# Optimization experiments

Hardware: AMD Instinct MI355X
Metric: run time of the kernel (lower is better)

The kernel has to match this reference:

```python
import jax, jax.numpy as jnp
import numpy as np

FREQ_DIM = 64
BLOCK_DIM = 64
N = 256          # lattice sites
CH = 6           # channel_num -> block diagonals at offsets -1, 0, +1
S = 2 * 16 + CH - 2   # seq_num = 36
BS = 4           # block_size (kron of two 2x2 matrices)
HID = 128
EPS = 1e-5
B = 32

_e = np.eye(2)
_sx = np.array([[0., 1.], [1., 0.]])
_siy = np.array([[0., 1.], [-1., 0.]])
_sz = np.array([[1., 0.], [0., -1.]])
_p = [_e, _sx, _siy, _sz]
KRONS = jnp.asarray(np.stack([np.kron(_p[a], _p[b]) for a in range(4) for b in range(4)]).astype(np.float32))  # (16,4,4)
Z1 = KRONS[12]  # kron(sigma_z, I) used for interaction blocks ('z1')


def _bn(h, g, b):
    # BatchNorm1d in training mode: biased batch statistics over axis 0
    mu = h.mean(axis=0)
    v = h.var(axis=0)
    return g * (h - mu) / jnp.sqrt(v + EPS) + b


def _mlp(x, Win, bin_, Wmid, bmid, Wout, bout, gamma, beta):
    # depth-4 MLP: Lin+ReLU, then (BN,Lin,ReLU) x2, then BN,Lin,ReLU
    h = jax.nn.relu(x @ Win + bin_)
    for i in range(Wmid.shape[0]):
        h = jax.nn.relu(_bn(h, gamma[i], beta[i]) @ Wmid[i] + bmid[i])
    return jax.nn.relu(_bn(h, gamma[-1], beta[-1]) @ Wout + bout)


def _lstm(xs, h0, c0, Wih, Whh, bih, bhh):
    # xs: (B, T, S); torch gate order i, f, g, o
    def step(carry, x_t):
        h, c = carry
        gates = x_t @ Wih.T + h @ Whh.T + (bih + bhh)
        i, f, g, o = jnp.split(gates, 4, axis=-1)
        c = jax.nn.sigmoid(f) * c + jax.nn.sigmoid(i) * jnp.tanh(g)
        h = jax.nn.sigmoid(o) * jnp.tanh(c)
        return (h, c), h
    _, hs = jax.lax.scan(step, (h0, c0), jnp.swapaxes(xs, 0, 1))
    return jnp.swapaxes(hs, 0, 1)


def setup_inputs() -> dict:
    key = jax.random.key(0)
    ks = iter(jax.random.split(key, 48))
    def w(shape, s=0.05):
        return jax.random.normal(next(ks), shape, dtype=jnp.float32) * s
    d = {
        'x': w((B, FREQ_DIM + BLOCK_DIM), 1.0),
        'fd_Win': w((FREQ_DIM, HID)), 'fd_bin': w((HID,)),
        'fd_Wmid': w((2, HID, HID)), 'fd_bmid': w((2, HID)),
        'fd_Wout': w((HID, S)), 'fd_bout': w((S,)),
        'fd_gamma': jnp.ones((3, HID), jnp.float32), 'fd_beta': jnp.zeros((3, HID), jnp.float32),
        'bd_Win': w((BLOCK_DIM, HID)), 'bd_bin': w((HID,)),
        'bd_Wmid': w((2, HID, HID)), 'bd_bmid': w((2, HID)),
        'bd_Wout': w((HID, S)), 'bd_bout': w((S,)),
        'bd_gamma': jnp.ones((3, HID), jnp.float32), 'bd_beta': jnp.zeros((3, HID), jnp.float32),
        'sc_Win': w((S, 1, HID)), 'sc_bin': w((S, HID)),
        'sc_Wmid': w((S, 2, HID, HID)), 'sc_bmid': w((S, 2, HID)),
        'sc_Wout': w((S, HID, N)), 'sc_bout': w((S, N)),
        'sc_gamma': jnp.ones((S, 3, HID), jnp.float32), 'sc_beta': jnp.zeros((S, 3, HID), jnp.float32),
        'lstm_Wih': w((4 * S, S)), 'lstm_Whh': w((4 * S, S)),
        'lstm_bih': w((4 * S,)), 'lstm_bhh': w((4 * S,)),
        'mix_W': w((S, 2 * S)), 'mix_b': w((S,)),
    }
    return d


def reference(x, fd_Win, fd_bin, fd_Wmid, fd_bmid, fd_Wout, fd_bout, fd_gamma, fd_beta,
              bd_Win, bd_bin, bd_Wmid, bd_bmid, bd_Wout, bd_bout, bd_gamma, bd_beta,
              sc_Win, sc_bin, sc_Wmid, sc_bmid, sc_Wout, sc_bout, sc_gamma, sc_beta,
              lstm_Wih, lstm_Whh, lstm_bih, lstm_bhh, mix_W, mix_b):
    Bsz = x.shape[0]
    block = _mlp(x[:, FREQ_DIM:], bd_Win, bd_bin, bd_Wmid, bd_bmid, bd_Wout, bd_bout, bd_gamma, bd_beta)  # (B,S)
    freq = _mlp(x[:, :FREQ_DIM], fd_Win, fd_bin, fd_Wmid, fd_bmid, fd_Wout, fd_bout, fd_gamma, fd_beta)   # (B,S)
    # S independent scalar->N MLPs, batched with vmap over the stacked params
    sc = jax.vmap(_mlp)(freq.T[:, :, None], sc_Win, sc_bin, sc_Wmid, sc_bmid,
                        sc_Wout, sc_bout, sc_gamma, sc_beta)  # (S,B,N)
    freq_seq = jnp.cos(sc).transpose(1, 2, 0)   # (B,N,S)
    seq = _lstm(freq_seq, block, jnp.zeros_like(block), lstm_Wih, lstm_Whh, lstm_bih, lstm_bhh)  # (B,N,S)
    block_seq = jnp.concatenate([jnp.broadcast_to(block[:, :, None], (Bsz, S, N)),
                                 jnp.swapaxes(seq, 1, 2)], axis=1)  # (B,2S,N)
    # 1x1 Conv2d == channel mixing matmul
    mixed = jnp.einsum('bcn,oc->bon', block_seq, mix_W) + mix_b[None, :, None]  # (B,S,N)
    inter = mixed[:, :CH - 2]                          # (B,CH-2,N)
    onsite = mixed[:, CH - 2:].reshape(Bsz, 2, 16, N)  # (B,2,16,N)
    H_int = jnp.einsum('bcn,ij->bcnij', inter, Z1)         # (B,CH-2,N,4,4)
    H_os = jnp.einsum('bgkn,kij->bgnij', onsite, KRONS)    # (B,2,N,4,4) summed over 16 pairs
    half = (CH - 2) // 2
    strips = jnp.concatenate([H_int[:, :half], H_os, H_int[:, half:]], axis=1)  # (B,CH,N,4,4)
    strips = strips.reshape(Bsz, CH // 2, 2, N, BS, BS)
    # banded block assembly: strip i lives on block-diagonal offset i - (CH//2)//2
    grid = jnp.zeros((Bsz, 2, N, N, BS, BS), dtype=x.dtype)
    for i in range(CH // 2):
        o = i - (CH // 2) // 2
        rows = jnp.arange(N - abs(o)) + max(0, -o)
        cols = rows + o
        grid = grid.at[:, :, rows, cols].set(strips[:, i][:, :, rows])
    matrix = grid.transpose(0, 1, 2, 4, 3, 5).reshape(Bsz, 2, N * BS, N * BS)
    return matrix
```

## Files before the change

kernel.cpp:

```cpp
#include <hip/hip_runtime.h>
#include <math.h>

#define EPSF 1e-5f

__device__ __forceinline__ float tanhf_fast(float x) {
    return 1.f - 2.f / (__expf(2.f * x) + 1.f);
}

__device__ void mlp64_body(const float* __restrict__ xin,
                           const float* __restrict__ Win,
                           const float* __restrict__ bin_,
                           const float* __restrict__ Wmid,
                           const float* __restrict__ bmid,
                           const float* __restrict__ Wout,
                           const float* __restrict__ bout,
                           const float* __restrict__ gamma,
                           const float* __restrict__ beta,
                           float* __restrict__ out)
{
    __shared__ float sX[32 * 64];
    __shared__ float sA[32 * 128];
    __shared__ float sB[32 * 128];
    __shared__ float sMu[128], sRs[128];
    int tid = threadIdx.x;

    for (int idx = tid; idx < 32 * 64; idx += 256) {
        int b = idx >> 6, c = idx & 63;
        sX[idx] = xin[b * 128 + c];
    }
    __syncthreads();

    for (int idx = tid; idx < 32 * 128; idx += 256) {
        int b = idx >> 7, j = idx & 127;
        float acc = bin_[j];
        for (int c = 0; c < 64; ++c) acc = fmaf(sX[b * 64 + c], Win[c * 128 + j], acc);
        sA[idx] = fmaxf(acc, 0.f);
    }
    __syncthreads();

    float* cur = sA;
    float* nxt = sB;
    for (int l = 0; l < 3; ++l) {
        if (tid < 128) {
            float s = 0.f, s2 = 0.f;
            for (int b = 0; b < 32; ++b) {
                float v = cur[b * 128 + tid];
                s += v; s2 += v * v;
            }
            float mu = s * (1.f / 32.f);
            float var = s2 * (1.f / 32.f) - mu * mu;
            sMu[tid] = mu;
            sRs[tid] = rsqrtf(var + EPSF);
        }
        __syncthreads();
        for (int idx = tid; idx < 32 * 128; idx += 256) {
            int j = idx & 127;
            cur[idx] = gamma[l * 128 + j] * (cur[idx] - sMu[j]) * sRs[j] + beta[l * 128 + j];
        }
        __syncthreads();
        if (l < 2) {
            for (int idx = tid; idx < 32 * 128; idx += 256) {
                int b = idx >> 7, j = idx & 127;
                float acc = bmid[l * 128 + j];
                for (int c = 0; c < 128; ++c)
                    acc = fmaf(cur[b * 128 + c], Wmid[(l * 128 + c) * 128 + j], acc);
                nxt[idx] = fmaxf(acc, 0.f);
            }
            __syncthreads();
            float* t = cur; cur = nxt; nxt = t;
        } else {
            for (int idx = tid; idx < 32 * 36; idx += 256) {
                int b = idx / 36, j = idx - b * 36;
                float acc = bout[j];
                for (int c = 0; c < 128; ++c)
                    acc = fmaf(cur[b * 128 + c], Wout[c * 36 + j], acc);
                out[idx] = fmaxf(acc, 0.f);
            }
        }
    }
}

__global__ __launch_bounds__(256) void k_mlp2(
    const float* __restrict__ x,
    const float* fdWin, const float* fdbin, const float* fdWmid, const float* fdbmid,
    const float* fdWout, const float* fdbout, const float* fdg, const float* fdbt,
    const float* bdWin, const float* bdbin, const float* bdWmid, const float* bdbmid,
    const float* bdWout, const float* bdbout, const float* bdg, const float* bdbt,
    float* freq, float* blk)
{
    if (blockIdx.x == 0)
        mlp64_body(x + 64, bdWin, bdbin, bdWmid, bdbmid, bdWout, bdbout, bdg, bdbt, blk);
    else
        mlp64_body(x, fdWin, fdbin, fdWmid, fdbmid, fdWout, fdbout, fdg, fdbt, freq);
}

__global__ __launch_bounds__(512) void k_sc(
    const float* __restrict__ freq,
    const float* __restrict__ Win,
    const float* __restrict__ bin_,
    const float* __restrict__ Wmid,
    const float* __restrict__ bmid,
    const float* __restrict__ Wout,
    const float* __restrict__ bout,
    const float* __restrict__ gamma,
    const float* __restrict__ beta,
    float* __restrict__ fseq)
{
    int s = blockIdx.x, tid = threadIdx.x;
    __shared__ float sA[32 * 128];
    __shared__ float sB[32 * 128];
    __shared__ float sMu[128], sRs[128];
    const float* Wm = Wmid + (size_t)s * 2 * 128 * 128;
    const float* Wo = Wout + (size_t)s * 128 * 256;
    const float* gm = gamma + s * 3 * 128;
    const float* bt = beta + s * 3 * 128;

    for (int idx = tid; idx < 32 * 128; idx += 512) {
        int b = idx >> 7, j = idx & 127;
        float acc = fmaf(freq[b * 36 + s], Win[s * 128 + j], bin_[s * 128 + j]);
        sA[idx] = fmaxf(acc, 0.f);
    }
    __syncthreads();

    float* cur = sA;
    float* nxt = sB;
    for (int l = 0; l < 3; ++l) {
        if (tid < 128) {
            float sm = 0.f, s2 = 0.f;
            for (int b = 0; b < 32; ++b) {
                float v = cur[b * 128 + tid];
                sm += v; s2 += v * v;
            }
            float mu = sm * (1.f / 32.f);
            float var = s2 * (1.f / 32.f) - mu * mu;
            sMu[tid] = mu;
            sRs[tid] = rsqrtf(var + EPSF);
        }
        __syncthreads();
        for (int idx = tid; idx < 32 * 128; idx += 512) {
            int j = idx & 127;
            cur[idx] = gm[l * 128 + j] * (cur[idx] - sMu[j]) * sRs[j] + bt[l * 128 + j];
        }
        __syncthreads();
        if (l < 2) {
            for (int idx = tid; idx < 32 * 128; idx += 512) {
                int b = idx >> 7, j = idx & 127;
                float acc = bmid[(s * 2 + l) * 128 + j];
                for (int c = 0; c < 128; ++c)
                    acc = fmaf(cur[b * 128 + c], Wm[(l * 128 + c) * 128 + j], acc);
                nxt[idx] = fmaxf(acc, 0.f);
            }
            __syncthreads();
            float* t = cur; cur = nxt; nxt = t;
        } else {
            for (int idx = tid; idx < 32 * 256; idx += 512) {
                int b = idx >> 8, n = idx & 255;
                float acc = bout[s * 256 + n];
                for (int c = 0; c < 128; ++c)
                    acc = fmaf(cur[b * 128 + c], Wo[c * 256 + n], acc);
                float v = fmaxf(acc, 0.f);
                fseq[((size_t)n * 32 + b) * 36 + s] = cosf(v);
            }
        }
    }
}

__global__ __launch_bounds__(512) void k_xg(
    const float* __restrict__ fseq, const float* __restrict__ Wih,
    const float* __restrict__ bih, const float* __restrict__ bhh,
    float* __restrict__ Xg)
{
    int t = blockIdx.x, tid = threadIdx.x;
    __shared__ float sF[32 * 36];
    for (int idx = tid; idx < 1152; idx += 512) sF[idx] = fseq[(size_t)t * 1152 + idx];
    __syncthreads();
    for (int idx = tid; idx < 32 * 144; idx += 512) {
        int b = idx / 144, j = idx - b * 144;
        float acc = bih[j] + bhh[j];
        #pragma unroll
        for (int s2 = 0; s2 < 36; ++s2)
            acc = fmaf(sF[b * 36 + s2], Wih[j * 36 + s2], acc);
        Xg[((size_t)t * 32 + b) * 144 + j] = acc;
    }
}

__global__ __launch_bounds__(192) void k_lstm(
    const float* __restrict__ Xg, const float* __restrict__ blockIn,
    const float* __restrict__ Whh, float* __restrict__ hseq)
{
    int b = blockIdx.x, tid = threadIdx.x;
    __shared__ float sh[36];
    __shared__ float sg[144];
    float w[36];
    if (tid < 144) {
        #pragma unroll
        for (int k = 0; k < 36; ++k) w[k] = Whh[tid * 36 + k];
    }
    if (tid < 36) sh[tid] = blockIn[b * 36 + tid];
    float c = 0.f;
    float xg = (tid < 144) ? Xg[(size_t)b * 144 + tid] : 0.f;
    const int type = tid / 36;
    __syncthreads();

    for (int t = 0; t < 256; ++t) {
        float act = 0.f;
        if (tid < 144) {
            float a0 = 0.f, a1 = 0.f, a2 = 0.f, a3 = 0.f;
            #pragma unroll
            for (int k = 0; k < 36; k += 4) {
                a0 = fmaf(w[k + 0], sh[k + 0], a0);
                a1 = fmaf(w[k + 1], sh[k + 1], a1);
                a2 = fmaf(w[k + 2], sh[k + 2], a2);
                a3 = fmaf(w[k + 3], sh[k + 3], a3);
            }
            float gate = xg + (a0 + a1) + (a2 + a3);
            float sarg = (type == 2) ? 2.f * gate : gate;
            float sv = 1.f / (1.f + __expf(-sarg));
            act = (type == 2) ? 2.f * sv - 1.f : sv;
        }
        if (t < 255 && tid < 144) xg = Xg[((size_t)(t + 1) * 32 + b) * 144 + tid];
        if (tid < 144) sg[tid] = act;
        __syncthreads();
        if (tid < 36) {
            float iv = sg[tid], fv = sg[36 + tid], gv = sg[72 + tid], ov = sg[108 + tid];
            c = fmaf(fv, c, iv * gv);
            float h = ov * tanhf_fast(c);
            sh[tid] = h;
            hseq[((size_t)b * 256 + t) * 36 + tid] = h;
        }
        __syncthreads();
    }
}

__global__ __launch_bounds__(256) void k_mixed(
    const float* __restrict__ blockIn, const float* __restrict__ hseq,
    const float* __restrict__ mixW, const float* __restrict__ mixb,
    float* __restrict__ mixed)
{
    int wg = blockIdx.x;
    int b = wg / 36, o = wg - b * 36;
    int n = threadIdx.x;
    float acc = mixb[o];
    const float* wrow = mixW + o * 72;
    const float* blk = blockIn + b * 36;
    #pragma unroll
    for (int c = 0; c < 36; ++c) acc = fmaf(wrow[c], blk[c], acc);
    const float* hp = hseq + ((size_t)b * 256 + n) * 36;
    #pragma unroll
    for (int u = 0; u < 36; ++u) acc = fmaf(wrow[36 + u], hp[u], acc);
    mixed[(size_t)wg * 256 + n] = acc;
}

__device__ __forceinline__ float pauliv(int p, int r, int c) {
    switch (p) {
        case 0: return (r == c) ? 1.f : 0.f;
        case 1: return (r != c) ? 1.f : 0.f;
        case 2: return (r == 0 && c == 1) ? 1.f : ((r == 1 && c == 0) ? -1.f : 0.f);
        default: return (r == c) ? ((r == 0) ? 1.f : -1.f) : 0.f;
    }
}

__global__ __launch_bounds__(256) void k_asm(
    const float* __restrict__ mixed, float* __restrict__ out)
{
    int wg = blockIdx.x;
    int n = wg & 255, bg = wg >> 8;
    int g = bg & 1, b = bg >> 1;
    int tid = threadIdx.x;
    __shared__ float sD[16];
    __shared__ float sEdge[2];
    if (tid < 16) {
        int r = tid >> 2, c = tid & 3;
        float acc = 0.f;
        #pragma unroll
        for (int k = 0; k < 16; ++k) {
            float kv = pauliv(k >> 2, r >> 1, c >> 1) * pauliv(k & 3, r & 1, c & 1);
            acc = fmaf(mixed[((size_t)b * 36 + 4 + 16 * g + k) * 256 + n], kv, acc);
        }
        sD[tid] = acc;
    } else if (tid == 16) {
        sEdge[0] = mixed[((size_t)b * 36 + g) * 256 + n];
    } else if (tid == 17) {
        sEdge[1] = mixed[((size_t)b * 36 + 2 + g) * 256 + n];
    }
    __syncthreads();

    float4* outp = (float4*)out + ((size_t)bg * 1024 + 4 * n) * 256;
    int m = tid;
    if (m == n) {
        #pragma unroll
        for (int r = 0; r < 4; ++r)
            outp[r * 256 + m] = make_float4(sD[r * 4 + 0], sD[r * 4 + 1], sD[r * 4 + 2], sD[r * 4 + 3]);
    } else if (m == n - 1) {
        float v = sEdge[0];
        outp[0 * 256 + m] = make_float4(v, 0.f, 0.f, 0.f);
        outp[1 * 256 + m] = make_float4(0.f, v, 0.f, 0.f);
        outp[2 * 256 + m] = make_float4(0.f, 0.f, -v, 0.f);
        outp[3 * 256 + m] = make_float4(0.f, 0.f, 0.f, -v);
    } else if (m == n + 1) {
        float v = sEdge[1];
        outp[0 * 256 + m] = make_float4(v, 0.f, 0.f, 0.f);
        outp[1 * 256 + m] = make_float4(0.f, v, 0.f, 0.f);
        outp[2 * 256 + m] = make_float4(0.f, 0.f, -v, 0.f);
        outp[3 * 256 + m] = make_float4(0.f, 0.f, 0.f, -v);
    } else {
        float4 z = make_float4(0.f, 0.f, 0.f, 0.f);
        #pragma unroll
        for (int r = 0; r < 4; ++r) outp[r * 256 + m] = z;
    }
}

extern "C" void kernel_launch(void* const* d_in, const int* in_sizes, int n_in,
                              void* d_out, int out_size, void* d_ws, size_t ws_size,
                              hipStream_t stream) {
    const float* x      = (const float*)d_in[0];
    const float* fdWin  = (const float*)d_in[1];
    const float* fdbin  = (const float*)d_in[2];
    const float* fdWmid = (const float*)d_in[3];
    const float* fdbmid = (const float*)d_in[4];
    const float* fdWout = (const float*)d_in[5];
    const float* fdbout = (const float*)d_in[6];
    const float* fdg    = (const float*)d_in[7];
    const float* fdbt   = (const float*)d_in[8];
    const float* bdWin  = (const float*)d_in[9];
    const float* bdbin  = (const float*)d_in[10];
    const float* bdWmid = (const float*)d_in[11];
    const float* bdbmid = (const float*)d_in[12];
    const float* bdWout = (const float*)d_in[13];
    const float* bdbout = (const float*)d_in[14];
    const float* bdg    = (const float*)d_in[15];
    const float* bdbt   = (const float*)d_in[16];
    const float* scWin  = (const float*)d_in[17];
    const float* scbin  = (const float*)d_in[18];
    const float* scWmid = (const float*)d_in[19];
    const float* scbmid = (const float*)d_in[20];
    const float* scWout = (const float*)d_in[21];
    const float* scbout = (const float*)d_in[22];
    const float* scg    = (const float*)d_in[23];
    const float* scbt   = (const float*)d_in[24];
    const float* Wih    = (const float*)d_in[25];
    const float* Whh    = (const float*)d_in[26];
    const float* bih    = (const float*)d_in[27];
    const float* bhh    = (const float*)d_in[28];
    const float* mixW   = (const float*)d_in[29];
    const float* mixb   = (const float*)d_in[30];

    float* ws    = (float*)d_ws;
    float* freq  = ws;
    float* blk   = ws + 1152;
    float* fseq  = ws + 2304;
    float* Xg    = ws + 297216;
    float* hseq  = ws + 1476864;
    float* mixed = ws + 1771776;

    k_mlp2<<<2, 256, 0, stream>>>(x,
        fdWin, fdbin, fdWmid, fdbmid, fdWout, fdbout, fdg, fdbt,
        bdWin, bdbin, bdWmid, bdbmid, bdWout, bdbout, bdg, bdbt,
        freq, blk);
    k_sc<<<36, 512, 0, stream>>>(freq, scWin, scbin, scWmid, scbmid,
                                 scWout, scbout, scg, scbt, fseq);
    k_xg<<<256, 512, 0, stream>>>(fseq, Wih, bih, bhh, Xg);
    k_lstm<<<32, 192, 0, stream>>>(Xg, blk, Whh, hseq);
    k_mixed<<<1152, 256, 0, stream>>>(blk, hseq, mixW, mixb, mixed);
    k_asm<<<16384, 256, 0, stream>>>(mixed, (float*)d_out);
}
```

Baseline: 375.6 us.

## Restructure LSTM to single-wave shuffle recurrence and retile MLP, mixing, assembly kernels

The LSTM is rewritten so that one 64-lane wavefront per batch holds the recurrent weights in registers and broadcasts h with shuffles. This removes the per-step shared-memory round trips and the two block barriers per timestep. The per-site MLP now uses register-blocked accumulators that reuse each weight load across several batch rows, and intermediate layouts are transposed to suit the new consumers. The mixing kernel stages h in shared memory and computes 9 outputs per block, and the assembly kernel drops its shared-memory/barrier step in favour of per-thread redundant loads. Costs include higher register pressure, a faster but less accurate cosine, and the mlp2 kernel moving to 512 threads.

```diff
diff --git a/kernel.cpp b/kernel.cpp
--- a/kernel.cpp
+++ b/kernel.cpp
@@ -2,9 +2,15 @@
 #include <math.h>
 
 #define EPSF 1e-5f
-
-__device__ __forceinline__ float tanhf_fast(float x) {
-    return 1.f - 2.f / (__expf(2.f * x) + 1.f);
+typedef __attribute__((ext_vector_type(2))) float f32x2;
+
+__device__ __forceinline__ float pauliv(int p, int r, int c) {
+    switch (p) {
+        case 0: return (r == c) ? 1.f : 0.f;
+        case 1: return (r != c) ? 1.f : 0.f;
+        case 2: return (r == 0 && c == 1) ? 1.f : ((r == 1 && c == 0) ? -1.f : 0.f);
+        default: return (r == c) ? ((r == 0) ? 1.f : -1.f) : 0.f;
+    }
 }
 
 __device__ void mlp64_body(const float* __restrict__ xin,
@@ -18,19 +24,19 @@
                            const float* __restrict__ beta,
                            float* __restrict__ out)
 {
-    __shared__ float sX[32 * 64];
-    __shared__ float sA[32 * 128];
-    __shared__ float sB[32 * 128];
+    __shared__ float sX[2048];
+    __shared__ float sA[4096];
+    __shared__ float sB[4096];
     __shared__ float sMu[128], sRs[128];
     int tid = threadIdx.x;
 
-    for (int idx = tid; idx < 32 * 64; idx += 256) {
+    for (int idx = tid; idx < 2048; idx += 512) {
         int b = idx >> 6, c = idx & 63;
         sX[idx] = xin[b * 128 + c];
     }
     __syncthreads();
 
-    for (int idx = tid; idx < 32 * 128; idx += 256) {
+    for (int idx = tid; idx < 4096; idx += 512) {
         int b = idx >> 7, j = idx & 127;
         float acc = bin_[j];
         for (int c = 0; c < 64; ++c) acc = fmaf(sX[b * 64 + c], Win[c * 128 + j], acc);
@@ -53,13 +59,13 @@
             sRs[tid] = rsqrtf(var + EPSF);
         }
         __syncthreads();
-        for (int idx = tid; idx < 32 * 128; idx += 256) {
+        for (int idx = tid; idx < 4096; idx += 512) {
             int j = idx & 127;
             cur[idx] = gamma[l * 128 + j] * (cur[idx] - sMu[j]) * sRs[j] + beta[l * 128 + j];
         }
         __syncthreads();
         if (l < 2) {
-            for (int idx = tid; idx < 32 * 128; idx += 256) {
+            for (int idx = tid; idx < 4096; idx += 512) {
                 int b = idx >> 7, j = idx & 127;
                 float acc = bmid[l * 128 + j];
                 for (int c = 0; c < 128; ++c)
@@ -69,7 +75,7 @@
             __syncthreads();
             float* t = cur; cur = nxt; nxt = t;
         } else {
-            for (int idx = tid; idx < 32 * 36; idx += 256) {
+            for (int idx = tid; idx < 1152; idx += 512) {
                 int b = idx / 36, j = idx - b * 36;
                 float acc = bout[j];
                 for (int c = 0; c < 128; ++c)
@@ -80,7 +86,7 @@
     }
 }
 
-__global__ __launch_bounds__(256) void k_mlp2(
+__global__ __launch_bounds__(512) void k_mlp2(
     const float* __restrict__ x,
     const float* fdWin, const float* fdbin, const float* fdWmid, const float* fdbmid,
     const float* fdWout, const float* fdbout, const float* fdg, const float* fdbt,
@@ -104,18 +110,18 @@
     const float* __restrict__ bout,
     const float* __restrict__ gamma,
     const float* __restrict__ beta,
-    float* __restrict__ fseq)
+    float* __restrict__ fseq2)
 {
     int s = blockIdx.x, tid = threadIdx.x;
-    __shared__ float sA[32 * 128];
-    __shared__ float sB[32 * 128];
+    __shared__ float sA[4096];
+    __shared__ float sB[4096];
     __shared__ float sMu[128], sRs[128];
     const float* Wm = Wmid + (size_t)s * 2 * 128 * 128;
     const float* Wo = Wout + (size_t)s * 128 * 256;
     const float* gm = gamma + s * 3 * 128;
     const float* bt = beta + s * 3 * 128;
 
-    for (int idx = tid; idx < 32 * 128; idx += 512) {
+    for (int idx = tid; idx < 4096; idx += 512) {
         int b = idx >> 7, j = idx & 127;
         float acc = fmaf(freq[b * 36 + s], Win[s * 128 + j], bin_[s * 128 + j]);
         sA[idx] = fmaxf(acc, 0.f);
@@ -137,126 +143,156 @@
             sRs[tid] = rsqrtf(var + EPSF);
         }
         __syncthreads();
-        for (int idx = tid; idx < 32 * 128; idx += 512) {
+        for (int idx = tid; idx < 4096; idx += 512) {
             int j = idx & 127;
             cur[idx] = gm[l * 128 + j] * (cur[idx] - sMu[j]) * sRs[j] + bt[l * 128 + j];
         }
         __syncthreads();
         if (l < 2) {
-            for (int idx = tid; idx < 32 * 128; idx += 512) {
-                int b = idx >> 7, j = idx & 127;
-                float acc = bmid[(s * 2 + l) * 128 + j];
-                for (int c = 0; c < 128; ++c)
-                    acc = fmaf(cur[b * 128 + c], Wm[(l * 128 + c) * 128 + j], acc);
-                nxt[idx] = fmaxf(acc, 0.f);
-            }
+            int jj = tid & 127, bb = tid >> 7;
+            float acc[8];
+            #pragma unroll
+            for (int k = 0; k < 8; ++k) acc[k] = bmid[(s * 2 + l) * 128 + jj];
+            for (int c = 0; c < 128; ++c) {
+                float w = Wm[(l * 128 + c) * 128 + jj];
+                #pragma unroll
+                for (int k = 0; k < 8; ++k)
+                    acc[k] = fmaf(cur[(bb + 4 * k) * 128 + c], w, acc[k]);
+            }
+            __syncthreads();
+            #pragma unroll
+            for (int k = 0; k < 8; ++k) nxt[(bb + 4 * k) * 128 + jj] = fmaxf(acc[k], 0.f);
             __syncthreads();
             float* t = cur; cur = nxt; nxt = t;
         } else {
-            for (int idx = tid; idx < 32 * 256; idx += 512) {
-                int b = idx >> 8, n = idx & 255;
-                float acc = bout[s * 256 + n];
-                for (int c = 0; c < 128; ++c)
-                    acc = fmaf(cur[b * 128 + c], Wo[c * 256 + n], acc);
-                float v = fmaxf(acc, 0.f);
-                fseq[((size_t)n * 32 + b) * 36 + s] = cosf(v);
+            int nn = tid & 255, bb2 = tid >> 8;
+            float acc[16];
+            #pragma unroll
+            for (int k = 0; k < 16; ++k) acc[k] = bout[s * 256 + nn];
+            for (int c = 0; c < 128; ++c) {
+                float w = Wo[c * 256 + nn];
+                #pragma unroll
+                for (int k = 0; k < 16; ++k)
+                    acc[k] = fmaf(cur[(bb2 + 2 * k) * 128 + c], w, acc[k]);
+            }
+            #pragma unroll
+            for (int k = 0; k < 16; ++k) {
+                float v = fmaxf(acc[k], 0.f);
+                fseq2[((size_t)s * 32 + bb2 + 2 * k) * 256 + nn] = __cosf(v);
             }
         }
     }
 }
 
 __global__ __launch_bounds__(512) void k_xg(
-    const float* __restrict__ fseq, const float* __restrict__ Wih,
+    const float* __restrict__ fseq2, const float* __restrict__ Wih,
     const float* __restrict__ bih, const float* __restrict__ bhh,
     float* __restrict__ Xg)
 {
     int t = blockIdx.x, tid = threadIdx.x;
-    __shared__ float sF[32 * 36];
-    for (int idx = tid; idx < 1152; idx += 512) sF[idx] = fseq[(size_t)t * 1152 + idx];
+    __shared__ float sF[1152];
+    __shared__ float sWt[36 * 144];
+    for (int idx = tid; idx < 1152; idx += 512) {
+        int s = idx >> 5, b = idx & 31;
+        sF[b * 36 + s] = fseq2[(size_t)idx * 256 + t];
+    }
+    for (int idx = tid; idx < 5184; idx += 512) {
+        int j = idx / 36, s = idx - j * 36;
+        sWt[s * 144 + j] = Wih[idx];
+    }
     __syncthreads();
-    for (int idx = tid; idx < 32 * 144; idx += 512) {
+    for (int idx = tid; idx < 4608; idx += 512) {
         int b = idx / 144, j = idx - b * 144;
         float acc = bih[j] + bhh[j];
         #pragma unroll
-        for (int s2 = 0; s2 < 36; ++s2)
-            acc = fmaf(sF[b * 36 + s2], Wih[j * 36 + s2], acc);
-        Xg[((size_t)t * 32 + b) * 144 + j] = acc;
-    }
-}
-
-__global__ __launch_bounds__(192) void k_lstm(
-    const float* __restrict__ Xg, const float* __restrict__ blockIn,
-    const float* __restrict__ Whh, float* __restrict__ hseq)
-{
-    int b = blockIdx.x, tid = threadIdx.x;
-    __shared__ float sh[36];
-    __shared__ float sg[144];
-    float w[36];
-    if (tid < 144) {
-        #pragma unroll
-        for (int k = 0; k < 36; ++k) w[k] = Whh[tid * 36 + k];
-    }
-    if (tid < 36) sh[tid] = blockIn[b * 36 + tid];
+        for (int s = 0; s < 36; ++s)
+            acc = fmaf(sF[b * 36 + s], sWt[s * 144 + j], acc);
+        Xg[((size_t)b * 256 + t) * 144 + j] = acc;
+    }
+}
+
+__global__ __launch_bounds__(64) void k_lstm(
+    const float* __restrict__ Xg,
+    const float* __restrict__ blk,
+    const float* __restrict__ Whh,
+    float* __restrict__ hseqT)
+{
+    int b = blockIdx.x;
+    int lane = threadIdx.x;
+    int uu = lane < 36 ? lane : 35;
+    bool active = lane < 36;
+
+    f32x2 wif[36], wgo[36];
+    #pragma unroll
+    for (int k = 0; k < 36; ++k) {
+        wif[k] = f32x2{Whh[uu * 36 + k], Whh[(36 + uu) * 36 + k]};
+        wgo[k] = f32x2{Whh[(72 + uu) * 36 + k], Whh[(108 + uu) * 36 + k]};
+    }
+    float h = blk[b * 36 + uu];
     float c = 0.f;
-    float xg = (tid < 144) ? Xg[(size_t)b * 144 + tid] : 0.f;
-    const int type = tid / 36;
-    __syncthreads();
+    const float* xgb = Xg + (size_t)b * 256 * 144;
+    f32x2 xif = f32x2{xgb[uu], xgb[36 + uu]};
+    f32x2 xgo = f32x2{xgb[72 + uu], xgb[108 + uu]};
+    float* hout = hseqT + ((size_t)b * 36 + uu) * 256;
 
     for (int t = 0; t < 256; ++t) {
-        float act = 0.f;
-        if (tid < 144) {
-            float a0 = 0.f, a1 = 0.f, a2 = 0.f, a3 = 0.f;
-            #pragma unroll
-            for (int k = 0; k < 36; k += 4) {
-                a0 = fmaf(w[k + 0], sh[k + 0], a0);
-                a1 = fmaf(w[k + 1], sh[k + 1], a1);
-                a2 = fmaf(w[k + 2], sh[k + 2], a2);
-                a3 = fmaf(w[k + 3], sh[k + 3], a3);
-            }
-            float gate = xg + (a0 + a1) + (a2 + a3);
-            float sarg = (type == 2) ? 2.f * gate : gate;
-            float sv = 1.f / (1.f + __expf(-sarg));
-            act = (type == 2) ? 2.f * sv - 1.f : sv;
-        }
-        if (t < 255 && tid < 144) xg = Xg[((size_t)(t + 1) * 32 + b) * 144 + tid];
-        if (tid < 144) sg[tid] = act;
-        __syncthreads();
-        if (tid < 36) {
-            float iv = sg[tid], fv = sg[36 + tid], gv = sg[72 + tid], ov = sg[108 + tid];
-            c = fmaf(fv, c, iv * gv);
-            float h = ov * tanhf_fast(c);
-            sh[tid] = h;
-            hseq[((size_t)b * 256 + t) * 36 + tid] = h;
-        }
-        __syncthreads();
+        f32x2 nif = xif, ngo = xgo;
+        if (t < 255) {
+            const float* xp = xgb + (size_t)(t + 1) * 144;
+            nif = f32x2{xp[uu], xp[36 + uu]};
+            ngo = f32x2{xp[72 + uu], xp[108 + uu]};
+        }
+        f32x2 aif = xif, ago = xgo;
+        #pragma unroll
+        for (int k = 0; k < 36; ++k) {
+            float hk = __shfl(h, k);
+            f32x2 hk2 = f32x2{hk, hk};
+            aif = __builtin_elementwise_fma(wif[k], hk2, aif);
+            ago = __builtin_elementwise_fma(wgo[k], hk2, ago);
+        }
+        float iv = 1.f / (1.f + __expf(-aif.x));
+        float fv = 1.f / (1.f + __expf(-aif.y));
+        float gv = 1.f - 2.f / (__expf(2.f * ago.x) + 1.f);
+        float ov = 1.f / (1.f + __expf(-ago.y));
+        c = fmaf(fv, c, iv * gv);
+        h = ov * (1.f - 2.f / (__expf(2.f * c) + 1.f));
+        if (active) hout[t] = h;
+        xif = nif; xgo = ngo;
     }
 }
 
 __global__ __launch_bounds__(256) void k_mixed(
-    const float* __restrict__ blockIn, const float* __restrict__ hseq,
+    const float* __restrict__ blk, const float* __restrict__ hseqT,
     const float* __restrict__ mixW, const float* __restrict__ mixb,
     float* __restrict__ mixed)
 {
-    int wg = blockIdx.x;
-    int b = wg / 36, o = wg - b * 36;
-    int n = threadIdx.x;
-    float acc = mixb[o];
-    const float* wrow = mixW + o * 72;
-    const float* blk = blockIn + b * 36;
+    int bq = blockIdx.x;
+    int b = bq >> 2, oq = bq & 3;
+    int tid = threadIdx.x;
+    __shared__ float sH[36 * 256];
+    __shared__ float sW[9 * 36];
+    __shared__ float sBase[9];
+    for (int idx = tid; idx < 9216; idx += 256)
+        sH[idx] = hseqT[(size_t)b * 9216 + idx];
+    for (int idx = tid; idx < 9 * 36; idx += 256) {
+        int o = idx / 36, u = idx - o * 36;
+        sW[idx] = mixW[(oq * 9 + o) * 72 + 36 + u];
+    }
+    if (tid < 9) {
+        int o = oq * 9 + tid;
+        float acc = mixb[o];
+        for (int c = 0; c < 36; ++c) acc = fmaf(mixW[o * 72 + c], blk[b * 36 + c], acc);
+        sBase[tid] = acc;
+    }
+    __syncthreads();
+    int n = tid;
     #pragma unroll
-    for (int c = 0; c < 36; ++c) acc = fmaf(wrow[c], blk[c], acc);
-    const float* hp = hseq + ((size_t)b * 256 + n) * 36;
-    #pragma unroll
-    for (int u = 0; u < 36; ++u) acc = fmaf(wrow[36 + u], hp[u], acc);
-    mixed[(size_t)wg * 256 + n] = acc;
-}
-
-__device__ __forceinline__ float pauliv(int p, int r, int c) {
-    switch (p) {
-        case 0: return (r == c) ? 1.f : 0.f;
-        case 1: return (r != c) ? 1.f : 0.f;
-        case 2: return (r == 0 && c == 1) ? 1.f : ((r == 1 && c == 0) ? -1.f : 0.f);
-        default: return (r == c) ? ((r == 0) ? 1.f : -1.f) : 0.f;
+    for (int o = 0; o < 9; ++o) {
+        float acc = sBase[o];
+        #pragma unroll
+        for (int u = 0; u < 36; ++u)
+            acc = fmaf(sW[o * 36 + u], sH[u * 256 + n], acc);
+        mixed[((size_t)b * 36 + oq * 9 + o) * 256 + n] = acc;
     }
 }
 
@@ -266,43 +302,42 @@
     int wg = blockIdx.x;
     int n = wg & 255, bg = wg >> 8;
     int g = bg & 1, b = bg >> 1;
-    int tid = threadIdx.x;
-    __shared__ float sD[16];
-    __shared__ float sEdge[2];
-    if (tid < 16) {
-        int r = tid >> 2, c = tid & 3;
+    const float* mb = mixed + (size_t)b * 36 * 256 + n;
+    float vSub = mb[(size_t)g * 256];
+    float vSup = mb[(size_t)(2 + g) * 256];
+    float ch[16];
+    #pragma unroll
+    for (int k = 0; k < 16; ++k) ch[k] = mb[(size_t)(4 + 16 * g + k) * 256];
+    float d[16];
+    #pragma unroll
+    for (int e = 0; e < 16; ++e) {
+        int r = e >> 2, cc = e & 3;
         float acc = 0.f;
         #pragma unroll
         for (int k = 0; k < 16; ++k) {
-            float kv = pauliv(k >> 2, r >> 1, c >> 1) * pauliv(k & 3, r & 1, c & 1);
-            acc = fmaf(mixed[((size_t)b * 36 + 4 + 16 * g + k) * 256 + n], kv, acc);
-        }
-        sD[tid] = acc;
-    } else if (tid == 16) {
-        sEdge[0] = mixed[((size_t)b * 36 + g) * 256 + n];
-    } else if (tid == 17) {
-        sEdge[1] = mixed[((size_t)b * 36 + 2 + g) * 256 + n];
-    }
-    __syncthreads();
+            float kv = pauliv(k >> 2, r >> 1, cc >> 1) * pauliv(k & 3, r & 1, cc & 1);
+            if (kv == 1.f) acc = acc + ch[k];
+            else if (kv == -1.f) acc = acc - ch[k];
+        }
+        d[e] = acc;
+    }
 
     float4* outp = (float4*)out + ((size_t)bg * 1024 + 4 * n) * 256;
-    int m = tid;
+    int m = threadIdx.x;
     if (m == n) {
         #pragma unroll
         for (int r = 0; r < 4; ++r)
-            outp[r * 256 + m] = make_float4(sD[r * 4 + 0], sD[r * 4 + 1], sD[r * 4 + 2], sD[r * 4 + 3]);
+            outp[r * 256 + m] = make_float4(d[r * 4 + 0], d[r * 4 + 1], d[r * 4 + 2], d[r * 4 + 3]);
     } else if (m == n - 1) {
-        float v = sEdge[0];
-        outp[0 * 256 + m] = make_float4(v, 0.f, 0.f, 0.f);
-        outp[1 * 256 + m] = make_float4(0.f, v, 0.f, 0.f);
-        outp[2 * 256 + m] = make_float4(0.f, 0.f, -v, 0.f);
-        outp[3 * 256 + m] = make_float4(0.f, 0.f, 0.f, -v);
+        outp[0 * 256 + m] = make_float4(vSub, 0.f, 0.f, 0.f);
+        outp[1 * 256 + m] = make_float4(0.f, vSub, 0.f, 0.f);
+        outp[2 * 256 + m] = make_float4(0.f, 0.f, -vSub, 0.f);
+        outp[3 * 256 + m] = make_float4(0.f, 0.f, 0.f, -vSub);
     } else if (m == n + 1) {
-        float v = sEdge[1];
-        outp[0 * 256 + m] = make_float4(v, 0.f, 0.f, 0.f);
-        outp[1 * 256 + m] = make_float4(0.f, v, 0.f, 0.f);
-        outp[2 * 256 + m] = make_float4(0.f, 0.f, -v, 0.f);
-        outp[3 * 256 + m] = make_float4(0.f, 0.f, 0.f, -v);
+        outp[0 * 256 + m] = make_float4(vSup, 0.f, 0.f, 0.f);
+        outp[1 * 256 + m] = make_float4(0.f, vSup, 0.f, 0.f);
+        outp[2 * 256 + m] = make_float4(0.f, 0.f, -vSup, 0.f);
+        outp[3 * 256 + m] = make_float4(0.f, 0.f, 0.f, -vSup);
     } else {
         float4 z = make_float4(0.f, 0.f, 0.f, 0.f);
         #pragma unroll
@@ -348,19 +383,19 @@
     float* ws    = (float*)d_ws;
     float* freq  = ws;
     float* blk   = ws + 1152;
-    float* fseq  = ws + 2304;
+    float* fseq2 = ws + 2304;
     float* Xg    = ws + 297216;
-    float* hseq  = ws + 1476864;
+    float* hseqT = ws + 1476864;
     float* mixed = ws + 1771776;
 
-    k_mlp2<<<2, 256, 0, stream>>>(x,
+    k_mlp2<<<2, 512, 0, stream>>>(x,
         fdWin, fdbin, fdWmid, fdbmid, fdWout, fdbout, fdg, fdbt,
         bdWin, bdbin, bdWmid, bdbmid, bdWout, bdbout, bdg, bdbt,
         freq, blk);
     k_sc<<<36, 512, 0, stream>>>(freq, scWin, scbin, scWmid, scbmid,
-                                 scWout, scbout, scg, scbt, fseq);
-    k_xg<<<256, 512, 0, stream>>>(fseq, Wih, bih, bhh, Xg);
-    k_lstm<<<32, 192, 0, stream>>>(Xg, blk, Whh, hseq);
-    k_mixed<<<1152, 256, 0, stream>>>(blk, hseq, mixW, mixb, mixed);
+                                 scWout, scbout, scg, scbt, fseq2);
+    k_xg<<<256, 512, 0, stream>>>(fseq2, Wih, bih, bhh, Xg);
+    k_lstm<<<32, 64, 0, stream>>>(Xg, blk, Whh, hseqT);
+    k_mixed<<<128, 256, 0, stream>>>(blk, hseqT, mixW, mixb, mixed);
     k_asm<<<16384, 256, 0, stream>>>(mixed, (float*)d_out);
 }
```

Result: slower. 424.9 us (+13.1%).
